# Performance work log

Hardware: AMD Instinct MI355X
Metric: run time of the kernel (lower is better)

Reference implementation:

```python
import jax, jax.numpy as jnp
import numpy as np

PI_APPROX = 3.1415926  # the source uses 3.1415926, not math.pi
N_RINGS = 10
N_ANGLES = 36  # k in range(0, 360, 10)


def setup_inputs() -> dict:
    key = jax.random.key(0)
    k1, k2, k3 = jax.random.split(key, 3)
    B, N = 32, 16384
    pred = jax.random.normal(k1, (B, N_RINGS), dtype=jnp.float32)
    target = jax.random.normal(k2, (B, N, 3), dtype=jnp.float32)
    trans_feat = jax.random.normal(k3, (B, 256), dtype=jnp.float32)
    return {"pred": pred, "target": target, "trans_feat": trans_feat}


def _generate_points(pred):
    # pred: [B, 10] radii. For ring j: center = [0.04, 0.15*j - 0.7, 0.0],
    # axis = y, firstPoint (centered) = [-r, 0, 0]. Rotating about y by angle a:
    # R @ [-r,0,0] = [-r*cos(a), 0, r*sin(a)]; then add center back.
    B = pred.shape[0]
    j = jnp.arange(N_RINGS, dtype=pred.dtype)
    cy = 0.15 * j - 0.7                                   # [10]
    ang = jnp.arange(0, 360, 10, dtype=pred.dtype) * (2.0 * PI_APPROX / 360.0)  # [36]
    c, s = jnp.cos(ang), jnp.sin(ang)
    r = pred[:, :, None]                                  # [B,10,1]
    px = -r * c[None, None, :] + 0.04                     # [B,10,36]
    py = jnp.broadcast_to(cy[None, :, None], px.shape)    # [B,10,36]
    pz = r * s[None, None, :]                             # [B,10,36]
    pts = jnp.stack([px, py, pz], axis=-1)                # [B,10,36,3]
    return pts.reshape(B, N_RINGS * N_ANGLES, 3)          # [B,360,3]


def reference(pred, target, trans_feat):
    B = pred.shape[0]
    pts = _generate_points(pred.reshape(B, N_RINGS))      # [B,360,3]
    # squared pairwise distances via ||a||^2 + ||b||^2 - 2 a.b
    d2 = (jnp.sum(pts * pts, axis=-1)[:, :, None]
          + jnp.sum(target * target, axis=-1)[:, None, :]
          - 2.0 * jnp.einsum('bpd,bnd->bpn', pts, target))  # [B,360,N]
    d2 = jnp.maximum(d2, 0.0)
    # original: min over target of ||pt - tgt||, then squared == min of squared dist
    min_d2 = jnp.min(d2, axis=-1)                         # [B,360]
    return jnp.mean(min_d2)
```

## Files before the change

### kernel.cpp

```cpp
#include <hip/hip_runtime.h>
#include <math.h>
#include <float.h>

#define N_RINGS  10
#define N_ANGLES 36
#define NP       (N_RINGS * N_ANGLES)
#define PI_APPROX 3.1415926f

#define BLOCK  256
#define WPB    4
#define CHUNK  1024
#define PPT    6

__global__ __launch_bounds__(BLOCK) void chamfer_minbuf(
    const float* __restrict__ pred,
    const float* __restrict__ target,
    unsigned int* __restrict__ minbuf,
    int N, int chunks)
{
    __shared__ float4 t4[CHUNK];
    __shared__ float  pm[WPB * NP];
    __shared__ float  cs_c[N_ANGLES], cs_s[N_ANGLES];

    const int b   = blockIdx.x / chunks;
    const int cg  = blockIdx.x % chunks;
    const int n0  = cg * CHUNK;
    const int tid = threadIdx.x;
    const int cnt = min(CHUNK, N - n0);

    if (tid < N_ANGLES) {
        float angf = (float)(10 * tid) * (2.0f * PI_APPROX / 360.0f);
        double ang = (double)angf;
        cs_c[tid] = (float)cos(ang);
        cs_s[tid] = (float)sin(ang);
    }
    for (int i = tid; i < cnt; i += BLOCK) {
        const float* t = target + ((size_t)b * N + (size_t)(n0 + i)) * 3;
        float x = t[0], y = t[1], z = t[2];
        t4[i] = make_float4(x, y, z, x * x + y * y + z * z);
    }
    __syncthreads();

    const int lane = tid & 63;
    const int w    = tid >> 6;

    float qx[PPT], qy[PPT], qz[PPT], pp2[PPT], m[PPT];
    #pragma unroll
    for (int k = 0; k < PPT; ++k) {
        int s = lane + 64 * k;
        int j = s / N_ANGLES;
        int a = s - j * N_ANGLES;
        int jc = (j < N_RINGS) ? j : (N_RINGS - 1);
        float r  = pred[b * N_RINGS + jc];
        float px = -r * cs_c[a] + 0.04f;
        float py = 0.15f * (float)jc - 0.7f;
        float pz = r * cs_s[a];
        pp2[k] = px * px + py * py + pz * pz;
        qx[k] = -2.0f * px;
        qy[k] = -2.0f * py;
        qz[k] = -2.0f * pz;
        m[k]  = FLT_MAX;
    }

    #pragma unroll 4
    for (int k = w; k < cnt; k += WPB) {
        float4 t = t4[k];
        #pragma unroll
        for (int i = 0; i < PPT; ++i) {
            float h = fmaf(qz[i], t.z, t.w);
            h = fmaf(qy[i], t.y, h);
            h = fmaf(qx[i], t.x, h);
            m[i] = fminf(m[i], h);
        }
    }

    #pragma unroll
    for (int k = 0; k < PPT; ++k) {
        int s = lane + 64 * k;
        if (s < NP) pm[w * NP + s] = fmaxf(pp2[k] + m[k], 0.0f);
    }
    __syncthreads();

    for (int p = tid; p < NP; p += BLOCK) {
        float v = fminf(fminf(pm[p], pm[NP + p]),
                        fminf(pm[2 * NP + p], pm[3 * NP + p]));
        atomicMin(&minbuf[b * NP + p], __float_as_uint(v));
    }
}

__global__ __launch_bounds__(1024) void reduce_mean(
    const unsigned int* __restrict__ minbuf, float* __restrict__ out,
    int count)
{
    __shared__ double sm[16];
    const int tid = threadIdx.x;
    double s = 0.0;
    for (int i = tid; i < count; i += 1024)
        s += (double)__uint_as_float(minbuf[i]);
    #pragma unroll
    for (int off = 32; off > 0; off >>= 1)
        s += __shfl_down(s, off, 64);
    if ((tid & 63) == 0) sm[tid >> 6] = s;
    __syncthreads();
    if (tid == 0) {
        double tot = 0.0;
        for (int wv = 0; wv < 16; ++wv) tot += sm[wv];
        out[0] = (float)(tot / (double)count);
    }
}

extern "C" void kernel_launch(void* const* d_in, const int* in_sizes, int n_in,
                              void* d_out, int out_size, void* d_ws, size_t ws_size,
                              hipStream_t stream) {
    const float* pred   = (const float*)d_in[0];
    const float* target = (const float*)d_in[1];

    const int B = in_sizes[0] / N_RINGS;
    const int N = in_sizes[1] / (3 * B);
    const int chunks = (N + CHUNK - 1) / CHUNK;
    const int count  = B * NP;

    unsigned int* minbuf = (unsigned int*)d_ws;
    float* out = (float*)d_out;

    hipMemsetAsync(minbuf, 0xFF, (size_t)count * sizeof(unsigned int), stream);

    hipLaunchKernelGGL(chamfer_minbuf, dim3(B * chunks), dim3(BLOCK), 0, stream,
                       pred, target, minbuf, N, chunks);
    hipLaunchKernelGGL(reduce_mean, dim3(1), dim3(1024), 0, stream,
                       minbuf, out, count);
}
```

Baseline: 85.89 us.

## Fuse min and mean reduction into one kernel with packed-FP32 distance loop

Replaces the atomicMin buffer and separate single-block mean kernel with per-chunk partial minima. The last block to finish for each batch reduces its chunks, and a packed fixed-point atomic counter lets the last batch write the mean, which removes one kernel launch and the large memset. The target tile is also stored in a pair-of-points SoA layout so the inner distance loop uses 2-wide float vector ops, intended to map to packed FP32 FMA. Costs include fixed-point quantization of the sum, extra threadfence/atomic sync, and a serial chunk loop in the last block.

```diff
diff --git a/kernel.cpp b/kernel.cpp
--- a/kernel.cpp
+++ b/kernel.cpp
@@ -4,7 +4,7 @@
 
 #define N_RINGS  10
 #define N_ANGLES 36
-#define NP       (N_RINGS * N_ANGLES)
+#define NP       360
 #define PI_APPROX 3.1415926f
 
 #define BLOCK  256
@@ -12,21 +12,30 @@
 #define CHUNK  1024
 #define PPT    6
 
-__global__ __launch_bounds__(BLOCK) void chamfer_minbuf(
+typedef float v2f __attribute__((ext_vector_type(2)));
+typedef unsigned long long ull;
+
+__global__ __launch_bounds__(BLOCK) void chamfer_fused(
     const float* __restrict__ pred,
     const float* __restrict__ target,
-    unsigned int* __restrict__ minbuf,
-    int N, int chunks)
+    float* __restrict__ part,
+    ull*  __restrict__ acc,
+    unsigned int* __restrict__ bcnt,
+    float* __restrict__ out,
+    int N, int chunks, int B)
 {
-    __shared__ float4 t4[CHUNK];
-    __shared__ float  pm[WPB * NP];
-    __shared__ float  cs_c[N_ANGLES], cs_s[N_ANGLES];
+    __shared__ v2f   tp[CHUNK / 2][4];
+    __shared__ float pm[WPB * NP];
+    __shared__ float cs_c[N_ANGLES], cs_s[N_ANGLES];
+    __shared__ double sd[WPB];
+    __shared__ int   sh_last;
 
     const int b   = blockIdx.x / chunks;
     const int cg  = blockIdx.x % chunks;
     const int n0  = cg * CHUNK;
     const int tid = threadIdx.x;
     const int cnt = min(CHUNK, N - n0);
+    const int cntp = (cnt + 1) & ~1;
 
     if (tid < N_ANGLES) {
         float angf = (float)(10 * tid) * (2.0f * PI_APPROX / 360.0f);
@@ -34,10 +43,15 @@
         cs_c[tid] = (float)cos(ang);
         cs_s[tid] = (float)sin(ang);
     }
-    for (int i = tid; i < cnt; i += BLOCK) {
-        const float* t = target + ((size_t)b * N + (size_t)(n0 + i)) * 3;
+    for (int i = tid; i < cntp; i += BLOCK) {
+        int ii = min(i, cnt - 1);
+        const float* t = target + ((size_t)b * N + (size_t)(n0 + ii)) * 3;
         float x = t[0], y = t[1], z = t[2];
-        t4[i] = make_float4(x, y, z, x * x + y * y + z * z);
+        int j = i >> 1, h = i & 1;
+        tp[j][0][h] = x;
+        tp[j][1][h] = y;
+        tp[j][2][h] = z;
+        tp[j][3][h] = x * x + y * y + z * z;
     }
     __syncthreads();
 
@@ -62,15 +76,16 @@
         m[k]  = FLT_MAX;
     }
 
-    #pragma unroll 4
-    for (int k = w; k < cnt; k += WPB) {
-        float4 t = t4[k];
+    const int pairs = cntp >> 1;
+    #pragma unroll 2
+    for (int k = w; k < pairs; k += WPB) {
+        v2f xv = tp[k][0], yv = tp[k][1], zv = tp[k][2], wv = tp[k][3];
         #pragma unroll
         for (int i = 0; i < PPT; ++i) {
-            float h = fmaf(qz[i], t.z, t.w);
-            h = fmaf(qy[i], t.y, h);
-            h = fmaf(qx[i], t.x, h);
-            m[i] = fminf(m[i], h);
+            v2f h = qz[i] * zv + wv;
+            h = qy[i] * yv + h;
+            h = qx[i] * xv + h;
+            m[i] = fminf(m[i], fminf(h.x, h.y));
         }
     }
 
@@ -84,28 +99,40 @@
     for (int p = tid; p < NP; p += BLOCK) {
         float v = fminf(fminf(pm[p], pm[NP + p]),
                         fminf(pm[2 * NP + p], pm[3 * NP + p]));
-        atomicMin(&minbuf[b * NP + p], __float_as_uint(v));
+        part[((size_t)b * chunks + cg) * NP + p] = v;
     }
-}
+    __threadfence();
+    __syncthreads();
+    if (tid == 0) {
+        unsigned int old = atomicAdd(&bcnt[b], 1u);
+        sh_last = (old == (unsigned int)(chunks - 1));
+    }
+    __syncthreads();
+    if (!sh_last) return;
 
-__global__ __launch_bounds__(1024) void reduce_mean(
-    const unsigned int* __restrict__ minbuf, float* __restrict__ out,
-    int count)
-{
-    __shared__ double sm[16];
-    const int tid = threadIdx.x;
-    double s = 0.0;
-    for (int i = tid; i < count; i += 1024)
-        s += (double)__uint_as_float(minbuf[i]);
+    __threadfence();
+    double lsum = 0.0;
+    const float* pb = part + (size_t)b * chunks * NP;
+    for (int p = tid; p < NP; p += BLOCK) {
+        float mn = pb[p];
+        for (int c = 1; c < chunks; ++c)
+            mn = fminf(mn, pb[(size_t)c * NP + p]);
+        lsum += (double)mn;
+    }
     #pragma unroll
     for (int off = 32; off > 0; off >>= 1)
-        s += __shfl_down(s, off, 64);
-    if ((tid & 63) == 0) sm[tid >> 6] = s;
+        lsum += __shfl_down(lsum, off, 64);
+    if ((tid & 63) == 0) sd[tid >> 6] = lsum;
     __syncthreads();
     if (tid == 0) {
-        double tot = 0.0;
-        for (int wv = 0; wv < 16; ++wv) tot += sm[wv];
-        out[0] = (float)(tot / (double)count);
+        double tot = sd[0] + sd[1] + sd[2] + sd[3];
+        ull fx   = (ull)(tot * 1073741824.0);
+        ull pack = fx | (1ULL << 56);
+        ull old  = atomicAdd(acc, pack);
+        if ((old >> 56) == (ull)(B - 1)) {
+            ull tfx = (old + pack) & ((1ULL << 56) - 1ULL);
+            out[0] = (float)((double)tfx / 1073741824.0 / (double)(B * NP));
+        }
     }
 }
 
@@ -118,15 +145,16 @@
     const int B = in_sizes[0] / N_RINGS;
     const int N = in_sizes[1] / (3 * B);
     const int chunks = (N + CHUNK - 1) / CHUNK;
-    const int count  = B * NP;
 
-    unsigned int* minbuf = (unsigned int*)d_ws;
+    float* part = (float*)d_ws;
+    size_t partBytes = (size_t)B * chunks * NP * sizeof(float);
+    ull* acc = (ull*)((char*)d_ws + partBytes);
+    unsigned int* bcnt = (unsigned int*)((char*)d_ws + partBytes + sizeof(ull));
     float* out = (float*)d_out;
 
-    hipMemsetAsync(minbuf, 0xFF, (size_t)count * sizeof(unsigned int), stream);
+    hipMemsetAsync((char*)d_ws + partBytes, 0,
+                   sizeof(ull) + (size_t)B * sizeof(unsigned int), stream);
 
-    hipLaunchKernelGGL(chamfer_minbuf, dim3(B * chunks), dim3(BLOCK), 0, stream,
-                       pred, target, minbuf, N, chunks);
-    hipLaunchKernelGGL(reduce_mean, dim3(1), dim3(1024), 0, stream,
-                       minbuf, out, count);
+    hipLaunchKernelGGL(chamfer_fused, dim3(B * chunks), dim3(BLOCK), 0, stream,
+                       pred, target, part, acc, bcnt, out, N, chunks, B);
 }
```

Result: slower. 125.5 us (+46.1%).

## Replace atomicMin minbuf with per-chunk partials and two-stage reduction

Applied to the files above, without the earlier changes.

Each block now writes its per-point minima into a per-(batch, chunk) partial buffer instead of doing global atomicMin, which removes the memset. A per-batch kernel then takes the min across chunks and sums, and a final kernel averages the batch sums. CHUNK is halved to 512, doubling the block count for more parallelism but also doubling the partial rows the reduction must scan. It adds one kernel launch and a serial loop over 32 chunks per point in batch_sum.

```diff
diff --git a/kernel.cpp b/kernel.cpp
--- a/kernel.cpp
+++ b/kernel.cpp
@@ -4,18 +4,18 @@
 
 #define N_RINGS  10
 #define N_ANGLES 36
-#define NP       (N_RINGS * N_ANGLES)
+#define NP       360
 #define PI_APPROX 3.1415926f
 
 #define BLOCK  256
 #define WPB    4
-#define CHUNK  1024
+#define CHUNK  512
 #define PPT    6
 
-__global__ __launch_bounds__(BLOCK) void chamfer_minbuf(
+__global__ __launch_bounds__(BLOCK) void chamfer_partial(
     const float* __restrict__ pred,
     const float* __restrict__ target,
-    unsigned int* __restrict__ minbuf,
+    float* __restrict__ part,
     int N, int chunks)
 {
     __shared__ float4 t4[CHUNK];
@@ -84,29 +84,45 @@
     for (int p = tid; p < NP; p += BLOCK) {
         float v = fminf(fminf(pm[p], pm[NP + p]),
                         fminf(pm[2 * NP + p], pm[3 * NP + p]));
-        atomicMin(&minbuf[b * NP + p], __float_as_uint(v));
+        part[((size_t)b * chunks + cg) * NP + p] = v;
     }
 }
 
-__global__ __launch_bounds__(1024) void reduce_mean(
-    const unsigned int* __restrict__ minbuf, float* __restrict__ out,
-    int count)
+__global__ __launch_bounds__(BLOCK) void batch_sum(
+    const float* __restrict__ part, double* __restrict__ ws2,
+    int chunks)
 {
-    __shared__ double sm[16];
+    __shared__ double sd[WPB];
+    const int b   = blockIdx.x;
     const int tid = threadIdx.x;
+    const float* pb = part + (size_t)b * chunks * NP;
+
     double s = 0.0;
-    for (int i = tid; i < count; i += 1024)
-        s += (double)__uint_as_float(minbuf[i]);
+    for (int p = tid; p < NP; p += BLOCK) {
+        float mn = pb[p];
+        for (int c = 1; c < chunks; ++c)
+            mn = fminf(mn, pb[(size_t)c * NP + p]);
+        s += (double)mn;
+    }
     #pragma unroll
     for (int off = 32; off > 0; off >>= 1)
         s += __shfl_down(s, off, 64);
-    if ((tid & 63) == 0) sm[tid >> 6] = s;
+    if ((tid & 63) == 0) sd[tid >> 6] = s;
     __syncthreads();
-    if (tid == 0) {
-        double tot = 0.0;
-        for (int wv = 0; wv < 16; ++wv) tot += sm[wv];
-        out[0] = (float)(tot / (double)count);
-    }
+    if (tid == 0)
+        ws2[b] = sd[0] + sd[1] + sd[2] + sd[3];
+}
+
+__global__ __launch_bounds__(64) void final_mean(
+    const double* __restrict__ ws2, float* __restrict__ out, int B)
+{
+    const int tid = threadIdx.x;
+    double s = (tid < B) ? ws2[tid] : 0.0;
+    #pragma unroll
+    for (int off = 32; off > 0; off >>= 1)
+        s += __shfl_down(s, off, 64);
+    if (tid == 0)
+        out[0] = (float)(s / (double)(B * NP));
 }
 
 extern "C" void kernel_launch(void* const* d_in, const int* in_sizes, int n_in,
@@ -118,15 +134,16 @@
     const int B = in_sizes[0] / N_RINGS;
     const int N = in_sizes[1] / (3 * B);
     const int chunks = (N + CHUNK - 1) / CHUNK;
-    const int count  = B * NP;
 
-    unsigned int* minbuf = (unsigned int*)d_ws;
+    float* part = (float*)d_ws;
+    size_t partBytes = (size_t)B * chunks * NP * sizeof(float);
+    double* ws2 = (double*)((char*)d_ws + partBytes);
     float* out = (float*)d_out;
 
-    hipMemsetAsync(minbuf, 0xFF, (size_t)count * sizeof(unsigned int), stream);
-
-    hipLaunchKernelGGL(chamfer_minbuf, dim3(B * chunks), dim3(BLOCK), 0, stream,
-                       pred, target, minbuf, N, chunks);
-    hipLaunchKernelGGL(reduce_mean, dim3(1), dim3(1024), 0, stream,
-                       minbuf, out, count);
+    hipLaunchKernelGGL(chamfer_partial, dim3(B * chunks), dim3(BLOCK), 0, stream,
+                       pred, target, part, N, chunks);
+    hipLaunchKernelGGL(batch_sum, dim3(B), dim3(BLOCK), 0, stream,
+                       part, ws2, chunks);
+    hipLaunchKernelGGL(final_mean, dim3(1), dim3(64), 0, stream,
+                       ws2, out, B);
 }
```

Measured after the change: 90.60 us. 1.05x slower.
